# Kernel optimization log

Measured on AMD Instinct MI355X. Metric: run time of the kernel, lower is better.

The kernel has to match this reference:

```python
import jax, jax.numpy as jnp
import numpy as np

H = 512
L = 4
A = 16
EPS = 1e-5


def setup_inputs() -> dict:
    key = jax.random.key(0)
    ks = jax.random.split(key, 16)
    B, S = 64, 256
    scale = 0.02
    inp = {
        "hidden": jnp.zeros((B, H), jnp.float32),
        "x": jax.random.normal(ks[0], (B, S, H), jnp.float32),
        "dones": jax.random.randint(ks[1], (B, S), 0, 2).astype(bool),
        "avail_actions": jax.random.randint(ks[2], (B, S, A), 0, 2).astype(bool),
        # MLP stack: L layers of Linear(H,H) + LayerNorm
        "Wl": jax.random.normal(ks[3], (L, H, H), jnp.float32) * scale,
        "bl": jnp.zeros((L, H), jnp.float32),
        "ln_g": jnp.ones((L, H), jnp.float32),
        "ln_b": jnp.zeros((L, H), jnp.float32),
        # GRUCell(H, H): torch layout weight_ih [3H, H] (r, z, n order)
        "W_ih": jax.random.normal(ks[4], (3 * H, H), jnp.float32) * scale,
        "W_hh": jax.random.normal(ks[5], (3 * H, H), jnp.float32) * scale,
        "b_ih": jnp.zeros((3 * H,), jnp.float32),
        "b_hh": jnp.zeros((3 * H,), jnp.float32),
        # output head
        "Wq": jax.random.normal(ks[6], (A, H), jnp.float32) * scale,
        "bq": jnp.zeros((A,), jnp.float32),
    }
    return inp


def _layer_norm(x, g, b):
    mu = jnp.mean(x, axis=-1, keepdims=True)
    var = jnp.mean(jnp.square(x - mu), axis=-1, keepdims=True)
    return (x - mu) * jax.lax.rsqrt(var + EPS) * g + b


def _gru_scan(h0, x, dones, W_ih, W_hh, b_ih, b_hh):
    # Precompute input projections for all timesteps: [B, S, 3H]
    gi = jnp.einsum("bsh,gh->bsg", x, W_ih) + b_ih
    gi_t = jnp.swapaxes(gi, 0, 1)          # [S, B, 3H]
    dones_t = jnp.swapaxes(dones, 0, 1)    # [S, B]

    def step(h, inputs):
        gi_s, done_s = inputs
        h = jnp.where(done_s[:, None], 0.0, h)  # reset carry where done
        gh = h @ W_hh.T + b_hh
        i_r, i_z, i_n = jnp.split(gi_s, 3, axis=-1)
        h_r, h_z, h_n = jnp.split(gh, 3, axis=-1)
        r = jax.nn.sigmoid(i_r + h_r)
        z = jax.nn.sigmoid(i_z + h_z)
        n = jnp.tanh(i_n + r * h_n)
        h_new = (1.0 - z) * n + z * h
        return h_new, h_new

    h_final, outs = jax.lax.scan(step, h0, (gi_t, dones_t))
    return h_final, jnp.swapaxes(outs, 0, 1)  # [B, S, H]


def reference(hidden, x, dones, avail_actions, Wl, bl, ln_g, ln_b,
              W_ih, W_hh, b_ih, b_hh, Wq, bq):
    h = x
    for l in range(L):
        h = jnp.einsum("bsh,oh->bso", h, Wl[l]) + bl[l]
        h = jax.nn.relu(_layer_norm(h, ln_g[l], ln_b[l]))
    hidden_out, rnn_out = _gru_scan(hidden, h, dones, W_ih, W_hh, b_ih, b_hh)
    q = jnp.einsum("bsh,ah->bsa", rnn_out, Wq) + bq
    unavail = 1.0 - avail_actions.astype(q.dtype)
    q = q - unavail * 1e10
    return hidden_out, q
```

## Files before the change

kernel.cpp:

```cpp
#include <hip/hip_runtime.h>
#include <hip/hip_bf16.h>

typedef short short8 __attribute__((ext_vector_type(8)));
typedef float f32x4 __attribute__((ext_vector_type(4)));

#define H 512
#define BATCH 64
#define SEQ 256
#define NROWS 16384
#define NDOM 16

__device__ __forceinline__ float bf2f(unsigned short u) {
    union { unsigned int i; float f; } v;
    v.i = ((unsigned int)u) << 16;
    return v.f;
}
__device__ __forceinline__ unsigned short f2bf(float f) {
    union { float f; unsigned int i; } v;
    v.f = f;
    unsigned int lsb = (v.i >> 16) & 1u;
    v.i += 0x7fffu + lsb;
    return (unsigned short)(v.i >> 16);
}
__device__ __forceinline__ float sigm(float x) { return 1.f / (1.f + __expf(-x)); }
__device__ __forceinline__ float tanh_fast(float x) { return 2.f / (1.f + __expf(-2.f * x)) - 1.f; }

__global__ __launch_bounds__(256) void cvt_init(
    const float* __restrict__ x, const float* __restrict__ Wl,
    const float* __restrict__ Wih,
    unsigned short* __restrict__ actA, unsigned short* __restrict__ wlb,
    unsigned short* __restrict__ wihb, unsigned int* __restrict__ meta)
{
    long idx4 = (long)blockIdx.x * 256 + threadIdx.x;
    if (idx4 < 2560) meta[idx4] = 0u;
    long i = idx4 * 4;
    const long N1 = 8388608;
    const long N2 = N1 + 1048576;
    const long N3 = N2 + 786432;
    const float* src; unsigned short* dst; long off;
    if (i < N1)      { src = x;   dst = actA; off = i; }
    else if (i < N2) { src = Wl;  dst = wlb;  off = i - N1; }
    else if (i < N3) { src = Wih; dst = wihb; off = i - N2; }
    else return;
    float4 v = *(const float4*)(src + off);
    ushort4 o;
    o.x = f2bf(v.x); o.y = f2bf(v.y); o.z = f2bf(v.z); o.w = f2bf(v.w);
    *(ushort4*)(dst + off) = o;
}

__global__ __launch_bounds__(256) void seg_build(
    const int* __restrict__ dones, int* __restrict__ lenArr,
    unsigned int* __restrict__ hist)
{
    __shared__ int d[256];
    const int b = blockIdx.x, s = threadIdx.x;
    d[s] = dones[b * 256 + s];
    __syncthreads();
    int len = 0;
    bool start = (s == 0) || (d[s] != 0);
    if (start) {
        len = 1;
        while (s + len < 256 && d[s + len] == 0) len++;
        atomicAdd(&hist[len], 1u);
    }
    lenArr[b * 256 + s] = len;
}

__global__ __launch_bounds__(256) void seg_offsets(
    const unsigned int* __restrict__ hist, int* __restrict__ Marr,
    unsigned int* __restrict__ offs, unsigned int* __restrict__ ssum)
{
    __shared__ unsigned int h[257];
    __shared__ int Msh[257];
    const int t = threadIdx.x;
    h[t] = hist[t];
    if (t == 0) h[256] = hist[256];
    __syncthreads();
    for (int tt = t; tt <= 256; tt += 256) {
        unsigned int m = 0;
        for (int L = tt + 1; L <= 256; ++L) m += h[L];
        Marr[tt] = (int)m;
        offs[tt] = m;
        Msh[tt] = (int)m;
    }
    __syncthreads();
    if (t == 0) {
        unsigned int acc = 0;
        for (int k = 0; k <= 256; ++k) { ssum[k] = acc; acc += (unsigned int)Msh[k]; }
    }
}

__global__ __launch_bounds__(256) void seg_scatter(
    const int* __restrict__ lenArr, unsigned int* __restrict__ offs,
    int* __restrict__ recs)
{
    const int b = blockIdx.x, s = threadIdx.x;
    int len = lenArr[b * 256 + s];
    if (len > 0) {
        unsigned int pos = atomicAdd(&offs[len], 1u);
        recs[pos] = (b << 16) | s;
    }
}

__global__ __launch_bounds__(256) void pmap_build(
    const int* __restrict__ recs, const int* __restrict__ Marr,
    const unsigned int* __restrict__ ssum, const int* __restrict__ lenArr,
    int* __restrict__ pmap)
{
    const int i = blockIdx.x * 256 + threadIdx.x;
    if (i >= Marr[0]) return;
    int rec = recs[i];
    int b = rec >> 16, st = rec & 0xffff;
    int len = lenArr[b * 256 + st];
    for (int t = 0; t < len; ++t) pmap[b * 256 + st + t] = (int)ssum[t] + i;
}

__global__ __launch_bounds__(256) void h_init(
    const int* __restrict__ recs, const int* __restrict__ Marr,
    const int* __restrict__ dones, const float* __restrict__ hidden,
    unsigned short* __restrict__ hst)
{
    const int w = threadIdx.x >> 6, lane = threadIdx.x & 63;
    const int i = blockIdx.x * 4 + w;
    const int nseg = Marr[0];
    const int c0 = lane * 8;
    unsigned short* dst = hst + (long)i * 512 + c0;
    if (i < nseg) {
        int rec = recs[i];
        int b = rec >> 16, st = rec & 0xffff;
        if (st == 0 && dones[b * 256] == 0) {
            float4 va = *(const float4*)(hidden + b * 512 + c0);
            float4 vb = *(const float4*)(hidden + b * 512 + c0 + 4);
            ushort4 o0 = {f2bf(va.x), f2bf(va.y), f2bf(va.z), f2bf(va.w)};
            ushort4 o1 = {f2bf(vb.x), f2bf(vb.y), f2bf(vb.z), f2bf(vb.w)};
            *(ushort4*)dst = o0; *(ushort4*)(dst + 4) = o1;
            return;
        }
    }
    ushort4 z4 = {0, 0, 0, 0};
    *(ushort4*)dst = z4; *(ushort4*)(dst + 4) = z4;
}

__global__ __launch_bounds__(256) void gemm_ln(
    const unsigned short* __restrict__ A,
    const unsigned short* __restrict__ W,
    const float* __restrict__ bias, const float* __restrict__ g,
    const float* __restrict__ b, unsigned short* __restrict__ Out)
{
    __shared__ unsigned short ldsA[64 * 64];
    __shared__ unsigned short ldsW[512 * 64];
    __shared__ float red[64 * 8];
    const int tid = threadIdx.x;
    const int lane = tid & 63;
    const int w = tid >> 6;
    const long m0 = (long)blockIdx.x * 64;

    f32x4 acc[4][8];
#pragma unroll
    for (int i = 0; i < 4; ++i)
#pragma unroll
        for (int jn = 0; jn < 8; ++jn) acc[i][jn] = (f32x4){0.f, 0.f, 0.f, 0.f};

    for (int kt = 0; kt < 512; kt += 64) {
        __syncthreads();
#pragma unroll
        for (int i = 0; i < 2; ++i) {
            int o = (i * 256 + tid) * 16;
            int row = o >> 7;
            int ch = (o & 127) >> 4;
            long gcol = (long)kt * 2 + (long)((ch ^ (row & 7)) << 4);
            __builtin_amdgcn_global_load_lds(
                (const unsigned int*)((const char*)A + (m0 + row) * 1024 + gcol),
                (unsigned int*)(ldsA + (i * 256 + w * 64) * 8), 16, 0, 0);
        }
#pragma unroll
        for (int i = 0; i < 16; ++i) {
            int o = (i * 256 + tid) * 16;
            int row = o >> 7;
            int ch = (o & 127) >> 4;
            long gcol = (long)kt * 2 + (long)((ch ^ (row & 7)) << 4);
            __builtin_amdgcn_global_load_lds(
                (const unsigned int*)((const char*)W + (long)row * 1024 + gcol),
                (unsigned int*)(ldsW + (i * 256 + w * 64) * 8), 16, 0, 0);
        }
        __syncthreads();

#pragma unroll
        for (int k2 = 0; k2 < 2; ++k2) {
            short8 af[4], bfr[8];
#pragma unroll
            for (int i = 0; i < 4; ++i) {
                int row = i * 16 + (lane & 15);
                int byteo = (row * 128 + k2 * 64 + ((lane >> 4) * 16)) ^ ((row & 7) << 4);
                af[i] = *(const short8*)((const char*)ldsA + byteo);
            }
#pragma unroll
            for (int jn = 0; jn < 8; ++jn) {
                int row = w * 128 + jn * 16 + (lane & 15);
                int byteo = (row * 128 + k2 * 64 + ((lane >> 4) * 16)) ^ ((row & 7) << 4);
                bfr[jn] = *(const short8*)((const char*)ldsW + byteo);
            }
#pragma unroll
            for (int i = 0; i < 4; ++i)
#pragma unroll
                for (int jn = 0; jn < 8; ++jn)
                    acc[i][jn] = __builtin_amdgcn_mfma_f32_16x16x32_bf16(af[i], bfr[jn], acc[i][jn], 0, 0, 0);
        }
    }

    float bz[8], gl[8], bl2[8];
#pragma unroll
    for (int jn = 0; jn < 8; ++jn) {
        int n = w * 128 + jn * 16 + (lane & 15);
        bz[jn] = bias[n]; gl[jn] = g[n]; bl2[jn] = b[n];
    }
#pragma unroll
    for (int i = 0; i < 4; ++i)
#pragma unroll
        for (int jn = 0; jn < 8; ++jn)
#pragma unroll
            for (int r = 0; r < 4; ++r) acc[i][jn][r] += bz[jn];

#pragma unroll
    for (int i = 0; i < 4; ++i) {
#pragma unroll
        for (int r = 0; r < 4; ++r) {
            float sv = 0.f, qv = 0.f;
#pragma unroll
            for (int jn = 0; jn < 8; ++jn) {
                float v = acc[i][jn][r];
                sv += v; qv += v * v;
            }
            sv += __shfl_xor(sv, 1); qv += __shfl_xor(qv, 1);
            sv += __shfl_xor(sv, 2); qv += __shfl_xor(qv, 2);
            sv += __shfl_xor(sv, 4); qv += __shfl_xor(qv, 4);
            sv += __shfl_xor(sv, 8); qv += __shfl_xor(qv, 8);
            if ((lane & 15) == 0) {
                int row = i * 16 + (lane >> 4) * 4 + r;
                red[row * 8 + w * 2] = sv;
                red[row * 8 + w * 2 + 1] = qv;
            }
        }
    }
    __syncthreads();

#pragma unroll
    for (int i = 0; i < 4; ++i) {
#pragma unroll
        for (int r = 0; r < 4; ++r) {
            int row = i * 16 + (lane >> 4) * 4 + r;
            float s_tot = red[row * 8 + 0] + red[row * 8 + 2] + red[row * 8 + 4] + red[row * 8 + 6];
            float q_tot = red[row * 8 + 1] + red[row * 8 + 3] + red[row * 8 + 5] + red[row * 8 + 7];
            float mu = s_tot * (1.f / 512.f);
            float var = q_tot * (1.f / 512.f) - mu * mu;
            float rs = rsqrtf(var + 1e-5f);
#pragma unroll
            for (int jn = 0; jn < 8; ++jn) {
                int n = w * 128 + jn * 16 + (lane & 15);
                float v = fmaxf(0.f, (acc[i][jn][r] - mu) * rs * gl[jn] + bl2[jn]);
                Out[(m0 + row) * 512 + n] = f2bf(v);
            }
        }
    }
}

__global__ __launch_bounds__(256) void gemm_bt(
    const unsigned short* __restrict__ A, const unsigned short* __restrict__ Bw,
    const float* __restrict__ bias, unsigned short* __restrict__ Cout,
    int M, int N, int K, const int* __restrict__ rowmap)
{
    __shared__ unsigned short ldsA[128 * 64];
    __shared__ unsigned short ldsB[128 * 64];
    const int tid = threadIdx.x;
    const int lane = tid & 63;
    const int w = tid >> 6;
    const int nbx = N >> 7;
    const int bm = blockIdx.x / nbx;
    const int bn = blockIdx.x % nbx;
    const long m0 = (long)bm * 128;
    const long n0 = (long)bn * 128;
    const long Kb = (long)K * 2;

    f32x4 acc[4][4];
#pragma unroll
    for (int i = 0; i < 4; ++i)
#pragma unroll
        for (int j = 0; j < 4; ++j) acc[i][j] = (f32x4){0.f, 0.f, 0.f, 0.f};

    for (int kt = 0; kt < K; kt += 64) {
        __syncthreads();
#pragma unroll
        for (int i = 0; i < 4; ++i) {
            int o   = (i * 256 + tid) * 16;
            int row = o >> 7;
            int ch  = (o & 127) >> 4;
            long gcol = (long)kt * 2 + (long)((ch ^ (row & 7)) << 4);
            int ldsoff = (i * 256 + w * 64) * 8;
            __builtin_amdgcn_global_load_lds(
                (const unsigned int*)((const char*)A + (m0 + row) * Kb + gcol),
                (unsigned int*)(ldsA + ldsoff), 16, 0, 0);
            __builtin_amdgcn_global_load_lds(
                (const unsigned int*)((const char*)Bw + (n0 + row) * Kb + gcol),
                (unsigned int*)(ldsB + ldsoff), 16, 0, 0);
        }
        __syncthreads();

#pragma unroll
        for (int k2 = 0; k2 < 2; ++k2) {
            short8 af[4], bfr[4];
#pragma unroll
            for (int i = 0; i < 4; ++i) {
                int row = (w >> 1) * 64 + i * 16 + (lane & 15);
                int byteo = (row * 128 + k2 * 64 + ((lane >> 4) * 16)) ^ ((row & 7) << 4);
                af[i] = *(const short8*)((const char*)ldsA + byteo);
            }
#pragma unroll
            for (int j = 0; j < 4; ++j) {
                int row = (w & 1) * 64 + j * 16 + (lane & 15);
                int byteo = (row * 128 + k2 * 64 + ((lane >> 4) * 16)) ^ ((row & 7) << 4);
                bfr[j] = *(const short8*)((const char*)ldsB + byteo);
            }
#pragma unroll
            for (int i = 0; i < 4; ++i)
#pragma unroll
                for (int j = 0; j < 4; ++j)
                    acc[i][j] = __builtin_amdgcn_mfma_f32_16x16x32_bf16(af[i], bfr[j], acc[i][j], 0, 0, 0);
        }
    }

#pragma unroll
    for (int j = 0; j < 4; ++j) {
        long n = n0 + (w & 1) * 64 + j * 16 + (lane & 15);
        float bz = bias ? bias[n] : 0.f;
#pragma unroll
        for (int i = 0; i < 4; ++i) {
#pragma unroll
            for (int r = 0; r < 4; ++r) {
                long m = m0 + (w >> 1) * 64 + i * 16 + (lane >> 4) * 4 + r;
                long mm = rowmap ? (long)rowmap[m] : m;
                Cout[mm * N + n] = f2bf(acc[i][j][r] + bz);
            }
        }
    }
}

__device__ __forceinline__ void dbar(unsigned int* __restrict__ dm,
                                     unsigned int epoch)
{
    __syncthreads();
    if (threadIdx.x == 0) {
        unsigned int p = __hip_atomic_fetch_add(&dm[0], 1u, __ATOMIC_RELAXED,
                                                __HIP_MEMORY_SCOPE_AGENT);
        if (p == (epoch + 1u) * 16u - 1u) {
            __hip_atomic_store(&dm[16], epoch + 1u, __ATOMIC_RELAXED,
                               __HIP_MEMORY_SCOPE_AGENT);
        } else {
            while (__hip_atomic_load(&dm[16], __ATOMIC_RELAXED,
                                     __HIP_MEMORY_SCOPE_AGENT) <= epoch)
                __builtin_amdgcn_s_sleep(2);
        }
    }
    __syncthreads();
    __builtin_amdgcn_sched_barrier(0);
}

__global__ __launch_bounds__(256, 1) void gru_seg_scan(
    const unsigned short* __restrict__ gi,
    const float* __restrict__ Whh,
    const float* __restrict__ bhh,
    const int* __restrict__ Marr,
    const unsigned int* __restrict__ ssum,
    const int* __restrict__ recs,
    unsigned short* __restrict__ hstA,
    unsigned short* __restrict__ hstB,
    unsigned short* __restrict__ rnn,
    float* __restrict__ hid_out,
    unsigned int* __restrict__ meta)
{
    __shared__ unsigned short ldsW[96 * 512];
    __shared__ int sMarr[257];
    __shared__ unsigned int sssum[257];
    const int tid = threadIdx.x;
    const int lane = tid & 63;
    const int w = tid >> 6;
    const int jg = blockIdx.x >> 4;
    const int dom = blockIdx.x & 15;
    const int j0 = jg * 32;

    for (int e = tid; e < 96 * 512; e += 256) {
        int rrow = e >> 9;
        int col = e & 511;
        int gate = rrow >> 5;
        int jl = rrow & 31;
        float v = Whh[((long)(gate * 512 + j0 + jl)) * 512 + col];
        int byteo = (rrow * 1024 + col * 2) ^ ((rrow & 7) << 4);
        *(unsigned short*)((char*)ldsW + byteo) = f2bf(v);
    }
    for (int e = tid; e < 257; e += 256) { sMarr[e] = Marr[e]; sssum[e] = ssum[e]; }

    const int jl16 = lane & 15;
    float bhr[2], bhz[2], bhn[2];
#pragma unroll
    for (int jj = 0; jj < 2; ++jj) {
        int jc = j0 + jj * 16 + jl16;
        bhr[jj] = bhh[jc]; bhz[jj] = bhh[512 + jc]; bhn[jj] = bhh[1024 + jc];
    }
    const int rbase = w * 16 + (lane >> 4) * 4;
    const int arowl = w * 16 + jl16;
    const int kcol0 = (lane >> 4) * 8;
    unsigned int* dmeta = meta + 64 * dom;
    __syncthreads();

    int crec[4], nrec[4];
    unsigned short cgr[4][2], cgz[4][2], cgn[4][2];
    unsigned short ngr[4][2], ngz[4][2], ngn[4][2];

    {
        const int Mt0 = sMarr[0];
        const long b0 = (long)sssum[0];
#pragma unroll
        for (int q = 0; q < 4; ++q) {
            int r = dom * 64 + rbase + q;
            if (r < Mt0) {
                crec[q] = recs[r];
#pragma unroll
                for (int jj = 0; jj < 2; ++jj) {
                    const unsigned short* gp = gi + (b0 + r) * 1536 + j0 + jj * 16 + jl16;
                    cgr[q][jj] = gp[0]; cgz[q][jj] = gp[512]; cgn[q][jj] = gp[1024];
                }
            } else crec[q] = -1;
        }
    }

    for (int t = 0; t < 256; ++t) {
        const int Mt = sMarr[t];
        if (Mt == 0) break;
        const int ntiles = (Mt + 63) >> 6;
        if (dom >= ntiles) break;
        const unsigned short* hsrc = (t & 1) ? hstB : hstA;
        unsigned short* hdst = (t & 1) ? hstA : hstB;
        const long base = (long)sssum[t];

        for (int tt = dom; tt < ntiles; tt += NDOM) {
            const int r0 = tt * 64;

            const unsigned short* arowp = hsrc + ((long)(r0 + arowl)) * 512 + kcol0;
            short8 af[16];
#pragma unroll
            for (int kk = 0; kk < 16; ++kk) {
                const unsigned short* ap = arowp + kk * 32;
                asm volatile("global_load_dwordx4 %0, %1, off sc0"
                             : "=v"(af[kk]) : "v"(ap));
            }
            unsigned int hu[4][2];
#pragma unroll
            for (int q = 0; q < 4; ++q)
#pragma unroll
                for (int jj = 0; jj < 2; ++jj) {
                    const unsigned short* hp = hsrc + (long)(r0 + rbase + q) * 512
                                             + j0 + jj * 16 + jl16;
                    asm volatile("global_load_ushort %0, %1, off sc0"
                                 : "=v"(hu[q][jj]) : "v"(hp));
                }
            asm volatile("s_waitcnt vmcnt(0)" ::: "memory");
            __builtin_amdgcn_sched_barrier(0);

            const bool instep = (tt + NDOM < ntiles);
            if (instep) {
#pragma unroll
                for (int q = 0; q < 4; ++q) {
                    int r = (tt + NDOM) * 64 + rbase + q;
                    if (r < Mt) {
                        nrec[q] = recs[r];
#pragma unroll
                        for (int jj = 0; jj < 2; ++jj) {
                            const unsigned short* gp = gi + (base + r) * 1536 + j0 + jj * 16 + jl16;
                            ngr[q][jj] = gp[0]; ngz[q][jj] = gp[512]; ngn[q][jj] = gp[1024];
                        }
                    } else nrec[q] = -1;
                }
            }

            f32x4 acch[3][2];
#pragma unroll
            for (int g = 0; g < 3; ++g)
#pragma unroll
                for (int jj = 0; jj < 2; ++jj) acch[g][jj] = (f32x4){0.f, 0.f, 0.f, 0.f};

#pragma unroll
            for (int kk = 0; kk < 16; ++kk) {
#pragma unroll
                for (int g = 0; g < 3; ++g)
#pragma unroll
                    for (int jj = 0; jj < 2; ++jj) {
                        int rrow = g * 32 + jj * 16 + jl16;
                        int bbyte = (rrow * 1024 + kk * 64 + ((lane >> 4) * 16)) ^ ((rrow & 7) << 4);
                        short8 bfrag = *(const short8*)((const char*)ldsW + bbyte);
                        acch[g][jj] = __builtin_amdgcn_mfma_f32_16x16x32_bf16(af[kk], bfrag, acch[g][jj], 0, 0, 0);
                    }
            }

#pragma unroll
            for (int q = 0; q < 4; ++q) {
                if (crec[q] >= 0) {
                    int r = r0 + rbase + q;
                    int b = crec[q] >> 16, st = crec[q] & 0xffff;
                    int s = st + t;
#pragma unroll
                    for (int jj = 0; jj < 2; ++jj) {
                        int jc = j0 + jj * 16 + jl16;
                        float heff = bf2f((unsigned short)hu[q][jj]);
                        float rgt = sigm(bf2f(cgr[q][jj]) + acch[0][jj][q] + bhr[jj]);
                        float zgt = sigm(bf2f(cgz[q][jj]) + acch[1][jj][q] + bhz[jj]);
                        float ngt = tanh_fast(bf2f(cgn[q][jj]) + rgt * (acch[2][jj][q] + bhn[jj]));
                        float hnew = (1.f - zgt) * ngt + zgt * heff;
                        unsigned short hb16 = f2bf(hnew);
                        hdst[(long)r * 512 + jc] = hb16;
                        rnn[((long)(b * 256 + s)) * 512 + jc] = hb16;
                        if (s == 255) hid_out[b * 512 + jc] = hnew;
                    }
                }
            }
            if (instep) {
#pragma unroll
                for (int q = 0; q < 4; ++q) {
                    crec[q] = nrec[q];
#pragma unroll
                    for (int jj = 0; jj < 2; ++jj) {
                        cgr[q][jj] = ngr[q][jj]; cgz[q][jj] = ngz[q][jj]; cgn[q][jj] = ngn[q][jj];
                    }
                }
            }
        }

        {
            const int Mt1 = sMarr[t + 1];
            if (Mt1 > 0 && dom < ((Mt1 + 63) >> 6)) {
                const long b1 = (long)sssum[t + 1];
#pragma unroll
                for (int q = 0; q < 4; ++q) {
                    int r = dom * 64 + rbase + q;
                    if (r < Mt1) {
                        crec[q] = recs[r];
#pragma unroll
                        for (int jj = 0; jj < 2; ++jj) {
                            const unsigned short* gp = gi + (b1 + r) * 1536 + j0 + jj * 16 + jl16;
                            cgr[q][jj] = gp[0]; cgz[q][jj] = gp[512]; cgn[q][jj] = gp[1024];
                        }
                    } else crec[q] = -1;
                }
            }
        }
        dbar(dmeta, (unsigned int)t);
    }
}

__global__ __launch_bounds__(256) void qhead(
    const unsigned short* __restrict__ rnn, const float* __restrict__ Wq,
    const float* __restrict__ bq, const int* __restrict__ avail,
    float* __restrict__ qout)
{
    const int w = threadIdx.x >> 6;
    const int lane = threadIdx.x & 63;
    const long row = (long)blockIdx.x * 4 + w;
    const int a = lane & 15;
    const int kc = lane >> 4;
    const unsigned short* hr = rnn + row * H + kc * 128;
    const float* wr = Wq + a * H + kc * 128;
    float sum = 0.f;
#pragma unroll
    for (int i = 0; i < 128; i += 8) {
        short8 hv = *(const short8*)(hr + i);
        float4 wa = *(const float4*)(wr + i);
        float4 wb = *(const float4*)(wr + i + 4);
        sum += bf2f((unsigned short)hv[0]) * wa.x;
        sum += bf2f((unsigned short)hv[1]) * wa.y;
        sum += bf2f((unsigned short)hv[2]) * wa.z;
        sum += bf2f((unsigned short)hv[3]) * wa.w;
        sum += bf2f((unsigned short)hv[4]) * wb.x;
        sum += bf2f((unsigned short)hv[5]) * wb.y;
        sum += bf2f((unsigned short)hv[6]) * wb.z;
        sum += bf2f((unsigned short)hv[7]) * wb.w;
    }
    sum += __shfl_xor(sum, 16);
    sum += __shfl_xor(sum, 32);
    if (kc == 0) {
        float qv = sum + bq[a];
        int av = avail[row * 16 + a];
        if (av == 0) qv -= 1e10f;
        qout[row * 16 + a] = qv;
    }
}

extern "C" void kernel_launch(void* const* d_in, const int* in_sizes, int n_in,
                              void* d_out, int out_size, void* d_ws, size_t ws_size,
                              hipStream_t stream)
{
    const float* hidden = (const float*)d_in[0];
    const float* x      = (const float*)d_in[1];
    const int*   dones  = (const int*)d_in[2];
    const int*   avail  = (const int*)d_in[3];
    const float* Wl     = (const float*)d_in[4];
    const float* bl     = (const float*)d_in[5];
    const float* ln_g   = (const float*)d_in[6];
    const float* ln_b   = (const float*)d_in[7];
    const float* W_ih   = (const float*)d_in[8];
    const float* W_hh   = (const float*)d_in[9];
    const float* b_ih   = (const float*)d_in[10];
    const float* b_hh   = (const float*)d_in[11];
    const float* Wq     = (const float*)d_in[12];
    const float* bq     = (const float*)d_in[13];

    char* p = (char*)d_ws;
    unsigned short* actA = (unsigned short*)p;
    unsigned short* hst0 = actA;
    p += (size_t)NROWS * H * 2;
    unsigned short* actB = (unsigned short*)p;
    unsigned short* gi   = actB;
    p += (size_t)NROWS * H * 2;
    p += (size_t)NROWS * H * 4;
    unsigned short* rnn  = (unsigned short*)p; p += (size_t)NROWS * H * 2;
    char* wreg = p;
    unsigned short* wlb  = (unsigned short*)wreg;
    unsigned short* wihb = (unsigned short*)(wreg + (size_t)4 * H * H * 2);
    unsigned short* hst1 = (unsigned short*)wreg;
    p += (size_t)NROWS * H * 2;
    int* lenArr = (int*)p;          p += (size_t)NROWS * 4;
    int* recs   = (int*)p;          p += (size_t)NROWS * 4;
    int* pmap   = (int*)p;          p += (size_t)NROWS * 4;
    unsigned int* meta = (unsigned int*)p;  p += 12288;
    unsigned int* hist = meta + 1024;
    unsigned int* offs = meta + 1296;
    int* Marr = (int*)(meta + 1568);
    unsigned int* ssum = meta + 1840;

    cvt_init<<<9984, 256, 0, stream>>>(x, Wl, W_ih, actA, wlb, wihb, meta);

    seg_build<<<64, 256, 0, stream>>>(dones, lenArr, hist);
    seg_offsets<<<1, 256, 0, stream>>>(hist, Marr, offs, ssum);
    seg_scatter<<<64, 256, 0, stream>>>(lenArr, offs, recs);
    pmap_build<<<64, 256, 0, stream>>>(recs, Marr, ssum, lenArr, pmap);

    unsigned short* cur = actA;
    unsigned short* nxt = actB;
    for (int l = 0; l < 4; ++l) {
        gemm_ln<<<256, 256, 0, stream>>>(cur, wlb + (size_t)l * H * H, bl + l * H,
                                         ln_g + l * H, ln_b + l * H, nxt);
        unsigned short* tsw = cur; cur = nxt; nxt = tsw;
    }

    gemm_bt<<<1536, 256, 0, stream>>>(cur, wihb, b_ih, gi, NROWS, 3 * H, H, pmap);

    h_init<<<4096, 256, 0, stream>>>(recs, Marr, dones, hidden, hst0);

    gru_seg_scan<<<256, 256, 0, stream>>>(gi, W_hh, b_hh, Marr, ssum, recs,
                                          hst0, hst1, rnn, (float*)d_out, meta);

    qhead<<<4096, 256, 0, stream>>>(rnn, Wq, bq, avail, (float*)d_out + BATCH * H);
}
```

Measured before the change: 584.3 us.

## Fuse MLP stack and GRU input projection into one LDS-resident kernel

Replaces the four per-layer gemm_ln launches and the separate gemm_bt input-projection launch with a single mlp_gi kernel. Each block keeps its 64-row activation tile in LDS across all layers and the W_ih projection, and converts x from fp32 to bf16 inline, so intermediate activations never go to global memory. The workspace is shrunk and h_init is limited to HSTCAP rows. The cost is a larger LDS footprint (about 64KB activations plus 64KB weights) and only 256 blocks, which lowers occupancy and parallelism for the projection stage.

```diff
diff --git a/kernel.cpp b/kernel.cpp
--- a/kernel.cpp
+++ b/kernel.cpp
@@ -9,6 +9,7 @@
 #define SEQ 256
 #define NROWS 16384
 #define NDOM 16
+#define HSTCAP 12288
 
 __device__ __forceinline__ float bf2f(unsigned short u) {
     union { unsigned int i; float f; } v;
@@ -26,21 +27,18 @@
 __device__ __forceinline__ float tanh_fast(float x) { return 2.f / (1.f + __expf(-2.f * x)) - 1.f; }
 
 __global__ __launch_bounds__(256) void cvt_init(
-    const float* __restrict__ x, const float* __restrict__ Wl,
-    const float* __restrict__ Wih,
-    unsigned short* __restrict__ actA, unsigned short* __restrict__ wlb,
-    unsigned short* __restrict__ wihb, unsigned int* __restrict__ meta)
+    const float* __restrict__ Wl, const float* __restrict__ Wih,
+    unsigned short* __restrict__ wlb, unsigned short* __restrict__ wihb,
+    unsigned int* __restrict__ meta)
 {
     long idx4 = (long)blockIdx.x * 256 + threadIdx.x;
     if (idx4 < 2560) meta[idx4] = 0u;
     long i = idx4 * 4;
-    const long N1 = 8388608;
-    const long N2 = N1 + 1048576;
-    const long N3 = N2 + 786432;
+    const long N1 = 1048576;
+    const long N2 = N1 + 786432;
     const float* src; unsigned short* dst; long off;
-    if (i < N1)      { src = x;   dst = actA; off = i; }
-    else if (i < N2) { src = Wl;  dst = wlb;  off = i - N1; }
-    else if (i < N3) { src = Wih; dst = wihb; off = i - N2; }
+    if (i < N1)      { src = Wl;  dst = wlb;  off = i; }
+    else if (i < N2) { src = Wih; dst = wihb; off = i - N1; }
     else return;
     float4 v = *(const float4*)(src + off);
     ushort4 o;
@@ -141,13 +139,18 @@
     *(ushort4*)dst = z4; *(ushort4*)(dst + 4) = z4;
 }
 
-__global__ __launch_bounds__(256) void gemm_ln(
-    const unsigned short* __restrict__ A,
-    const unsigned short* __restrict__ W,
-    const float* __restrict__ bias, const float* __restrict__ g,
-    const float* __restrict__ b, unsigned short* __restrict__ Out)
-{
-    __shared__ unsigned short ldsA[64 * 64];
+__global__ __launch_bounds__(256) void mlp_gi(
+    const float* __restrict__ x,
+    const unsigned short* __restrict__ wlb,
+    const unsigned short* __restrict__ wihb,
+    const float* __restrict__ bl,
+    const float* __restrict__ lng,
+    const float* __restrict__ lnb,
+    const float* __restrict__ bih,
+    const int* __restrict__ pmap,
+    unsigned short* __restrict__ gi)
+{
+    __shared__ unsigned short ldsAct[64 * 512];
     __shared__ unsigned short ldsW[512 * 64];
     __shared__ float red[64 * 8];
     const int tid = threadIdx.x;
@@ -155,191 +158,185 @@
     const int w = tid >> 6;
     const long m0 = (long)blockIdx.x * 64;
 
-    f32x4 acc[4][8];
+#pragma unroll
+    for (int it = 0; it < 16; ++it) {
+        int ch = it * 256 + tid;
+        int row = ch >> 6;
+        int c = ch & 63;
+        const float* xp = x + (m0 + row) * 512 + c * 8;
+        float4 a = *(const float4*)xp;
+        float4 b4 = *(const float4*)(xp + 4);
+        short8 v;
+        v[0] = (short)f2bf(a.x);  v[1] = (short)f2bf(a.y);
+        v[2] = (short)f2bf(a.z);  v[3] = (short)f2bf(a.w);
+        v[4] = (short)f2bf(b4.x); v[5] = (short)f2bf(b4.y);
+        v[6] = (short)f2bf(b4.z); v[7] = (short)f2bf(b4.w);
+        int byteo = (row * 1024 + c * 16) ^ ((row & 7) << 4);
+        *(short8*)((char*)ldsAct + byteo) = v;
+    }
+    int pm[4][4];
 #pragma unroll
     for (int i = 0; i < 4; ++i)
 #pragma unroll
-        for (int jn = 0; jn < 8; ++jn) acc[i][jn] = (f32x4){0.f, 0.f, 0.f, 0.f};
-
-    for (int kt = 0; kt < 512; kt += 64) {
+        for (int r = 0; r < 4; ++r)
+            pm[i][r] = pmap[m0 + i * 16 + (lane >> 4) * 4 + r];
+    __syncthreads();
+
+    for (int l = 0; l < 4; ++l) {
+        const unsigned short* W = wlb + (long)l * 512 * 512;
+        f32x4 acc[4][8];
+#pragma unroll
+        for (int i = 0; i < 4; ++i)
+#pragma unroll
+            for (int jn = 0; jn < 8; ++jn) acc[i][jn] = (f32x4){0.f, 0.f, 0.f, 0.f};
+
+        for (int kt = 0; kt < 512; kt += 64) {
+            __syncthreads();
+#pragma unroll
+            for (int i = 0; i < 16; ++i) {
+                int o = (i * 256 + tid) * 16;
+                int row = o >> 7;
+                int c = (o & 127) >> 4;
+                long gcol = (long)kt * 2 + (long)((c ^ (row & 7)) << 4);
+                __builtin_amdgcn_global_load_lds(
+                    (const unsigned int*)((const char*)W + (long)row * 1024 + gcol),
+                    (unsigned int*)(ldsW + (i * 256 + w * 64) * 8), 16, 0, 0);
+            }
+            __syncthreads();
+#pragma unroll
+            for (int k2 = 0; k2 < 2; ++k2) {
+                short8 af[4], bfr[8];
+#pragma unroll
+                for (int i = 0; i < 4; ++i) {
+                    int row = i * 16 + (lane & 15);
+                    int byteo = (row * 1024 + kt * 2 + k2 * 64 + ((lane >> 4) * 16)) ^ ((row & 7) << 4);
+                    af[i] = *(const short8*)((const char*)ldsAct + byteo);
+                }
+#pragma unroll
+                for (int jn = 0; jn < 8; ++jn) {
+                    int row = w * 128 + jn * 16 + (lane & 15);
+                    int byteo = (row * 128 + k2 * 64 + ((lane >> 4) * 16)) ^ ((row & 7) << 4);
+                    bfr[jn] = *(const short8*)((const char*)ldsW + byteo);
+                }
+#pragma unroll
+                for (int i = 0; i < 4; ++i)
+#pragma unroll
+                    for (int jn = 0; jn < 8; ++jn)
+                        acc[i][jn] = __builtin_amdgcn_mfma_f32_16x16x32_bf16(af[i], bfr[jn], acc[i][jn], 0, 0, 0);
+            }
+        }
+
+        float bz[8], gl[8], bb[8];
+#pragma unroll
+        for (int jn = 0; jn < 8; ++jn) {
+            int n = w * 128 + jn * 16 + (lane & 15);
+            bz[jn] = bl[l * 512 + n]; gl[jn] = lng[l * 512 + n]; bb[jn] = lnb[l * 512 + n];
+        }
+#pragma unroll
+        for (int i = 0; i < 4; ++i)
+#pragma unroll
+            for (int jn = 0; jn < 8; ++jn)
+#pragma unroll
+                for (int r = 0; r < 4; ++r) acc[i][jn][r] += bz[jn];
+
+#pragma unroll
+        for (int i = 0; i < 4; ++i) {
+#pragma unroll
+            for (int r = 0; r < 4; ++r) {
+                float sv = 0.f, qv = 0.f;
+#pragma unroll
+                for (int jn = 0; jn < 8; ++jn) {
+                    float v = acc[i][jn][r];
+                    sv += v; qv += v * v;
+                }
+                sv += __shfl_xor(sv, 1); qv += __shfl_xor(qv, 1);
+                sv += __shfl_xor(sv, 2); qv += __shfl_xor(qv, 2);
+                sv += __shfl_xor(sv, 4); qv += __shfl_xor(qv, 4);
+                sv += __shfl_xor(sv, 8); qv += __shfl_xor(qv, 8);
+                if ((lane & 15) == 0) {
+                    int row = i * 16 + (lane >> 4) * 4 + r;
+                    red[row * 8 + w * 2] = sv;
+                    red[row * 8 + w * 2 + 1] = qv;
+                }
+            }
+        }
         __syncthreads();
-#pragma unroll
-        for (int i = 0; i < 2; ++i) {
-            int o = (i * 256 + tid) * 16;
-            int row = o >> 7;
-            int ch = (o & 127) >> 4;
-            long gcol = (long)kt * 2 + (long)((ch ^ (row & 7)) << 4);
-            __builtin_amdgcn_global_load_lds(
-                (const unsigned int*)((const char*)A + (m0 + row) * 1024 + gcol),
-                (unsigned int*)(ldsA + (i * 256 + w * 64) * 8), 16, 0, 0);
-        }
-#pragma unroll
-        for (int i = 0; i < 16; ++i) {
-            int o = (i * 256 + tid) * 16;
-            int row = o >> 7;
-            int ch = (o & 127) >> 4;
-            long gcol = (long)kt * 2 + (long)((ch ^ (row & 7)) << 4);
-            __builtin_amdgcn_global_load_lds(
-                (const unsigned int*)((const char*)W + (long)row * 1024 + gcol),
-                (unsigned int*)(ldsW + (i * 256 + w * 64) * 8), 16, 0, 0);
+
+#pragma unroll
+        for (int i = 0; i < 4; ++i) {
+#pragma unroll
+            for (int r = 0; r < 4; ++r) {
+                int row = i * 16 + (lane >> 4) * 4 + r;
+                float s_tot = red[row * 8 + 0] + red[row * 8 + 2] + red[row * 8 + 4] + red[row * 8 + 6];
+                float q_tot = red[row * 8 + 1] + red[row * 8 + 3] + red[row * 8 + 5] + red[row * 8 + 7];
+                float mu = s_tot * (1.f / 512.f);
+                float var = q_tot * (1.f / 512.f) - mu * mu;
+                float rs = rsqrtf(var + 1e-5f);
+#pragma unroll
+                for (int jn = 0; jn < 8; ++jn) {
+                    int col = w * 128 + jn * 16 + (lane & 15);
+                    float v = fmaxf(0.f, (acc[i][jn][r] - mu) * rs * gl[jn] + bb[jn]);
+                    int byteo = (row * 1024 + col * 2) ^ ((row & 7) << 4);
+                    *(unsigned short*)((char*)ldsAct + byteo) = f2bf(v);
+                }
+            }
         }
         __syncthreads();
-
-#pragma unroll
-        for (int k2 = 0; k2 < 2; ++k2) {
-            short8 af[4], bfr[8];
-#pragma unroll
-            for (int i = 0; i < 4; ++i) {
-                int row = i * 16 + (lane & 15);
-                int byteo = (row * 128 + k2 * 64 + ((lane >> 4) * 16)) ^ ((row & 7) << 4);
-                af[i] = *(const short8*)((const char*)ldsA + byteo);
-            }
-#pragma unroll
-            for (int jn = 0; jn < 8; ++jn) {
-                int row = w * 128 + jn * 16 + (lane & 15);
-                int byteo = (row * 128 + k2 * 64 + ((lane >> 4) * 16)) ^ ((row & 7) << 4);
-                bfr[jn] = *(const short8*)((const char*)ldsW + byteo);
-            }
+    }
+
+    for (int nc = 0; nc < 3; ++nc) {
+        const unsigned short* W = wihb + (long)nc * 512 * 512;
+        f32x4 acc[4][8];
+#pragma unroll
+        for (int i = 0; i < 4; ++i)
+#pragma unroll
+            for (int jn = 0; jn < 8; ++jn) acc[i][jn] = (f32x4){0.f, 0.f, 0.f, 0.f};
+
+        for (int kt = 0; kt < 512; kt += 64) {
+            __syncthreads();
+#pragma unroll
+            for (int i = 0; i < 16; ++i) {
+                int o = (i * 256 + tid) * 16;
+                int row = o >> 7;
+                int c = (o & 127) >> 4;
+                long gcol = (long)kt * 2 + (long)((c ^ (row & 7)) << 4);
+                __builtin_amdgcn_global_load_lds(
+                    (const unsigned int*)((const char*)W + (long)row * 1024 + gcol),
+                    (unsigned int*)(ldsW + (i * 256 + w * 64) * 8), 16, 0, 0);
+            }
+            __syncthreads();
+#pragma unroll
+            for (int k2 = 0; k2 < 2; ++k2) {
+                short8 af[4], bfr[8];
+#pragma unroll
+                for (int i = 0; i < 4; ++i) {
+                    int row = i * 16 + (lane & 15);
+                    int byteo = (row * 1024 + kt * 2 + k2 * 64 + ((lane >> 4) * 16)) ^ ((row & 7) << 4);
+                    af[i] = *(const short8*)((const char*)ldsAct + byteo);
+                }
+#pragma unroll
+                for (int jn = 0; jn < 8; ++jn) {
+                    int row = w * 128 + jn * 16 + (lane & 15);
+                    int byteo = (row * 128 + k2 * 64 + ((lane >> 4) * 16)) ^ ((row & 7) << 4);
+                    bfr[jn] = *(const short8*)((const char*)ldsW + byteo);
+                }
+#pragma unroll
+                for (int i = 0; i < 4; ++i)
+#pragma unroll
+                    for (int jn = 0; jn < 8; ++jn)
+                        acc[i][jn] = __builtin_amdgcn_mfma_f32_16x16x32_bf16(af[i], bfr[jn], acc[i][jn], 0, 0, 0);
+            }
+        }
+
+#pragma unroll
+        for (int jn = 0; jn < 8; ++jn) {
+            int colg = nc * 512 + w * 128 + jn * 16 + (lane & 15);
+            float bz = bih[colg];
 #pragma unroll
             for (int i = 0; i < 4; ++i)
 #pragma unroll
-                for (int jn = 0; jn < 8; ++jn)
-                    acc[i][jn] = __builtin_amdgcn_mfma_f32_16x16x32_bf16(af[i], bfr[jn], acc[i][jn], 0, 0, 0);
-        }
-    }
-
-    float bz[8], gl[8], bl2[8];
-#pragma unroll
-    for (int jn = 0; jn < 8; ++jn) {
-        int n = w * 128 + jn * 16 + (lane & 15);
-        bz[jn] = bias[n]; gl[jn] = g[n]; bl2[jn] = b[n];
-    }
-#pragma unroll
-    for (int i = 0; i < 4; ++i)
-#pragma unroll
-        for (int jn = 0; jn < 8; ++jn)
-#pragma unroll
-            for (int r = 0; r < 4; ++r) acc[i][jn][r] += bz[jn];
-
-#pragma unroll
-    for (int i = 0; i < 4; ++i) {
-#pragma unroll
-        for (int r = 0; r < 4; ++r) {
-            float sv = 0.f, qv = 0.f;
-#pragma unroll
-            for (int jn = 0; jn < 8; ++jn) {
-                float v = acc[i][jn][r];
-                sv += v; qv += v * v;
-            }
-            sv += __shfl_xor(sv, 1); qv += __shfl_xor(qv, 1);
-            sv += __shfl_xor(sv, 2); qv += __shfl_xor(qv, 2);
-            sv += __shfl_xor(sv, 4); qv += __shfl_xor(qv, 4);
-            sv += __shfl_xor(sv, 8); qv += __shfl_xor(qv, 8);
-            if ((lane & 15) == 0) {
-                int row = i * 16 + (lane >> 4) * 4 + r;
-                red[row * 8 + w * 2] = sv;
-                red[row * 8 + w * 2 + 1] = qv;
-            }
-        }
-    }
-    __syncthreads();
-
-#pragma unroll
-    for (int i = 0; i < 4; ++i) {
-#pragma unroll
-        for (int r = 0; r < 4; ++r) {
-            int row = i * 16 + (lane >> 4) * 4 + r;
-            float s_tot = red[row * 8 + 0] + red[row * 8 + 2] + red[row * 8 + 4] + red[row * 8 + 6];
-            float q_tot = red[row * 8 + 1] + red[row * 8 + 3] + red[row * 8 + 5] + red[row * 8 + 7];
-            float mu = s_tot * (1.f / 512.f);
-            float var = q_tot * (1.f / 512.f) - mu * mu;
-            float rs = rsqrtf(var + 1e-5f);
-#pragma unroll
-            for (int jn = 0; jn < 8; ++jn) {
-                int n = w * 128 + jn * 16 + (lane & 15);
-                float v = fmaxf(0.f, (acc[i][jn][r] - mu) * rs * gl[jn] + bl2[jn]);
-                Out[(m0 + row) * 512 + n] = f2bf(v);
-            }
-        }
-    }
-}
-
-__global__ __launch_bounds__(256) void gemm_bt(
-    const unsigned short* __restrict__ A, const unsigned short* __restrict__ Bw,
-    const float* __restrict__ bias, unsigned short* __restrict__ Cout,
-    int M, int N, int K, const int* __restrict__ rowmap)
-{
-    __shared__ unsigned short ldsA[128 * 64];
-    __shared__ unsigned short ldsB[128 * 64];
-    const int tid = threadIdx.x;
-    const int lane = tid & 63;
-    const int w = tid >> 6;
-    const int nbx = N >> 7;
-    const int bm = blockIdx.x / nbx;
-    const int bn = blockIdx.x % nbx;
-    const long m0 = (long)bm * 128;
-    const long n0 = (long)bn * 128;
-    const long Kb = (long)K * 2;
-
-    f32x4 acc[4][4];
-#pragma unroll
-    for (int i = 0; i < 4; ++i)
-#pragma unroll
-        for (int j = 0; j < 4; ++j) acc[i][j] = (f32x4){0.f, 0.f, 0.f, 0.f};
-
-    for (int kt = 0; kt < K; kt += 64) {
-        __syncthreads();
-#pragma unroll
-        for (int i = 0; i < 4; ++i) {
-            int o   = (i * 256 + tid) * 16;
-            int row = o >> 7;
-            int ch  = (o & 127) >> 4;
-            long gcol = (long)kt * 2 + (long)((ch ^ (row & 7)) << 4);
-            int ldsoff = (i * 256 + w * 64) * 8;
-            __builtin_amdgcn_global_load_lds(
-                (const unsigned int*)((const char*)A + (m0 + row) * Kb + gcol),
-                (unsigned int*)(ldsA + ldsoff), 16, 0, 0);
-            __builtin_amdgcn_global_load_lds(
-                (const unsigned int*)((const char*)Bw + (n0 + row) * Kb + gcol),
-                (unsigned int*)(ldsB + ldsoff), 16, 0, 0);
-        }
-        __syncthreads();
-
-#pragma unroll
-        for (int k2 = 0; k2 < 2; ++k2) {
-            short8 af[4], bfr[4];
-#pragma unroll
-            for (int i = 0; i < 4; ++i) {
-                int row = (w >> 1) * 64 + i * 16 + (lane & 15);
-                int byteo = (row * 128 + k2 * 64 + ((lane >> 4) * 16)) ^ ((row & 7) << 4);
-                af[i] = *(const short8*)((const char*)ldsA + byteo);
-            }
-#pragma unroll
-            for (int j = 0; j < 4; ++j) {
-                int row = (w & 1) * 64 + j * 16 + (lane & 15);
-                int byteo = (row * 128 + k2 * 64 + ((lane >> 4) * 16)) ^ ((row & 7) << 4);
-                bfr[j] = *(const short8*)((const char*)ldsB + byteo);
-            }
-#pragma unroll
-            for (int i = 0; i < 4; ++i)
-#pragma unroll
-                for (int j = 0; j < 4; ++j)
-                    acc[i][j] = __builtin_amdgcn_mfma_f32_16x16x32_bf16(af[i], bfr[j], acc[i][j], 0, 0, 0);
-        }
-    }
-
-#pragma unroll
-    for (int j = 0; j < 4; ++j) {
-        long n = n0 + (w & 1) * 64 + j * 16 + (lane & 15);
-        float bz = bias ? bias[n] : 0.f;
-#pragma unroll
-        for (int i = 0; i < 4; ++i) {
-#pragma unroll
-            for (int r = 0; r < 4; ++r) {
-                long m = m0 + (w >> 1) * 64 + i * 16 + (lane >> 4) * 4 + r;
-                long mm = rowmap ? (long)rowmap[m] : m;
-                Cout[mm * N + n] = f2bf(acc[i][j][r] + bz);
-            }
+                for (int r = 0; r < 4; ++r)
+                    gi[(long)pm[i][r] * 1536 + colg] = f2bf(acc[i][jn][r] + bz);
         }
     }
 }
@@ -612,19 +609,12 @@
     const float* bq     = (const float*)d_in[13];
 
     char* p = (char*)d_ws;
-    unsigned short* actA = (unsigned short*)p;
-    unsigned short* hst0 = actA;
-    p += (size_t)NROWS * H * 2;
-    unsigned short* actB = (unsigned short*)p;
-    unsigned short* gi   = actB;
-    p += (size_t)NROWS * H * 2;
-    p += (size_t)NROWS * H * 4;
+    unsigned short* gi   = (unsigned short*)p; p += (size_t)NROWS * 1536 * 2;
     unsigned short* rnn  = (unsigned short*)p; p += (size_t)NROWS * H * 2;
-    char* wreg = p;
-    unsigned short* wlb  = (unsigned short*)wreg;
-    unsigned short* wihb = (unsigned short*)(wreg + (size_t)4 * H * H * 2);
-    unsigned short* hst1 = (unsigned short*)wreg;
-    p += (size_t)NROWS * H * 2;
+    unsigned short* hst0 = (unsigned short*)p; p += (size_t)HSTCAP * H * 2;
+    unsigned short* hst1 = (unsigned short*)p; p += (size_t)HSTCAP * H * 2;
+    unsigned short* wlb  = (unsigned short*)p; p += (size_t)4 * H * H * 2;
+    unsigned short* wihb = (unsigned short*)p; p += (size_t)3 * H * H * 2;
     int* lenArr = (int*)p;          p += (size_t)NROWS * 4;
     int* recs   = (int*)p;          p += (size_t)NROWS * 4;
     int* pmap   = (int*)p;          p += (size_t)NROWS * 4;
@@ -634,24 +624,16 @@
     int* Marr = (int*)(meta + 1568);
     unsigned int* ssum = meta + 1840;
 
-    cvt_init<<<9984, 256, 0, stream>>>(x, Wl, W_ih, actA, wlb, wihb, meta);
+    cvt_init<<<1792, 256, 0, stream>>>(Wl, W_ih, wlb, wihb, meta);
 
     seg_build<<<64, 256, 0, stream>>>(dones, lenArr, hist);
     seg_offsets<<<1, 256, 0, stream>>>(hist, Marr, offs, ssum);
     seg_scatter<<<64, 256, 0, stream>>>(lenArr, offs, recs);
     pmap_build<<<64, 256, 0, stream>>>(recs, Marr, ssum, lenArr, pmap);
 
-    unsigned short* cur = actA;
-    unsigned short* nxt = actB;
-    for (int l = 0; l < 4; ++l) {
-        gemm_ln<<<256, 256, 0, stream>>>(cur, wlb + (size_t)l * H * H, bl + l * H,
-                                         ln_g + l * H, ln_b + l * H, nxt);
-        unsigned short* tsw = cur; cur = nxt; nxt = tsw;
-    }
-
-    gemm_bt<<<1536, 256, 0, stream>>>(cur, wihb, b_ih, gi, NROWS, 3 * H, H, pmap);
-
-    h_init<<<4096, 256, 0, stream>>>(recs, Marr, dones, hidden, hst0);
+    h_init<<<HSTCAP / 4, 256, 0, stream>>>(recs, Marr, dones, hidden, hst0);
+
+    mlp_gi<<<256, 256, 0, stream>>>(x, wlb, wihb, bl, ln_g, ln_b, b_ih, pmap, gi);
 
     gru_seg_scan<<<256, 256, 0, stream>>>(gi, W_hh, b_hh, Marr, ssum, recs,
                                           hst0, hst1, rnn, (float*)d_out, meta);
```

After: 572.7 us. 2.0% less time.
